# Kernel optimization log

Measured on AMD Instinct MI355X. Metric: run time of the kernel, lower is better.

The kernel has to match this reference:

```python
import math
import jax, jax.numpy as jnp
import numpy as np


def _sinkhorn_attn(q, n):
    """Log-domain Sinkhorn-Knopp, eps=1, max_iter=1, uniform marginals.
    cost C = -q @ q^T, so M = (-C + u + v)/eps = S + u + v with S = q q^T.
    Returns transport plan pi = exp(S + u_i + v_j).  q: [B, n, d]."""
    S = jnp.einsum('bnd,bmd->bnm', q, q)            # [B, n, n]
    log_marg = -math.log(n)                          # log(1/n)
    u = log_marg - jax.nn.logsumexp(S, axis=-1)      # [B, n] row update
    v = log_marg - jax.nn.logsumexp(S + u[..., :, None], axis=-2)  # [B, n] col update
    return jnp.exp(S + u[..., :, None] + v[..., None, :])


def reference(x, row_embed, col_embed):
    # x: [B, d, H, W]; row_embed/col_embed: [len_embedding, d//2]
    B, d, H, W = x.shape
    # learned positional embedding: [H, W, d] -> [d, H, W]
    x_emb = col_embed[:W]                             # [W, F]
    y_emb = row_embed[:H]                             # [H, F]
    F = x_emb.shape[-1]
    pos = jnp.concatenate([
        jnp.broadcast_to(x_emb[None, :, :], (H, W, F)),
        jnp.broadcast_to(y_emb[:, None, :], (H, W, F)),
    ], axis=-1).transpose(2, 0, 1)                    # [d, H, W]
    x = x + pos[None]

    n = H * W
    xf = x.reshape(B, d, n).transpose(0, 2, 1)        # [B, n, d] = q = k = v (v unscaled)
    inv_sqrtV = 1.0 / math.sqrt(math.sqrt(d))         # d**-0.25 applied to q and k each
    attn = _sinkhorn_attn(xf * inv_sqrtV, n)          # [B, n, n]
    out = jnp.einsum('bnm,bmd->bnd', attn, xf)        # [B, n, d]
    return out.transpose(0, 2, 1).reshape(B, d, H, W)


def setup_inputs() -> dict:
    key = jax.random.key(0)
    k1, k2, k3 = jax.random.split(key, 3)
    B, d, H, W = 32, 512, 32, 32
    len_emb, F = 32, d // 2
    return {
        'x': jax.random.normal(k1, (B, d, H, W), dtype=jnp.float32),
        'row_embed': jax.random.uniform(k2, (len_emb, F), dtype=jnp.float32),
        'col_embed': jax.random.uniform(k3, (len_emb, F), dtype=jnp.float32),
    }
```

## Files before the change

kernel.cpp:

```cpp
#include <hip/hip_runtime.h>
#include <hip/hip_fp16.h>
#include <math.h>

typedef _Float16 f16;
typedef _Float16 f16x8 __attribute__((ext_vector_type(8)));
typedef _Float16 f16x4 __attribute__((ext_vector_type(4)));
typedef float f32x4 __attribute__((ext_vector_type(4)));

namespace {
constexpr int kB = 32, kD = 512, kN = 1024, kF = 256;
constexpr float kScale = 0.04419417382415922f;
constexpr float kLogMarg = -6.931471805599453f;
constexpr float kMarg = 1.f / 1024.f;
constexpr float kPScale = 16384.f;
constexpr float kPInv = 1.f / 16384.f;
}

__device__ __forceinline__ void gload16(const void* g, void* l) {
  __builtin_amdgcn_global_load_lds(
      (const __attribute__((address_space(1))) void*)g,
      (__attribute__((address_space(3))) void*)l, 16, 0, 0);
}

__global__ __launch_bounds__(256) void k_prep(
    const float* __restrict__ x, const float* __restrict__ re,
    const float* __restrict__ ce, f16* __restrict__ xf,
    f16* __restrict__ xfT, int b0) {
  __shared__ f16 T[64][68];
  const int lb = blockIdx.z;
  const int i0 = blockIdx.x * 64, c0 = blockIdx.y * 64;
  const int t = threadIdx.x;
  const int il = (t & 15) * 4;
  const int cl = t >> 4;
  const size_t xbase = ((size_t)(b0 + lb) * kD) * kN;
#pragma unroll
  for (int p = 0; p < 4; p++) {
    const int c = c0 + cl + 16 * p;
    const int i = i0 + il;
    const float4 xv = *(const float4*)(x + xbase + (size_t)c * kN + i);
    float4 pv;
    if (c < kF) {
      pv.x = ce[((i + 0) & 31) * kF + c];
      pv.y = ce[((i + 1) & 31) * kF + c];
      pv.z = ce[((i + 2) & 31) * kF + c];
      pv.w = ce[((i + 3) & 31) * kF + c];
    } else {
      const float r = re[(i >> 5) * kF + (c - kF)];
      pv.x = r; pv.y = r; pv.z = r; pv.w = r;
    }
    const f16 h0 = (f16)(xv.x + pv.x), h1 = (f16)(xv.y + pv.y);
    const f16 h2 = (f16)(xv.z + pv.z), h3 = (f16)(xv.w + pv.w);
    f16* dT = xfT + ((size_t)lb * kD + c) * kN + i;
    *(f16x4*)dT = (f16x4){h0, h1, h2, h3};
    T[cl + 16 * p][il + 0] = h0; T[cl + 16 * p][il + 1] = h1;
    T[cl + 16 * p][il + 2] = h2; T[cl + 16 * p][il + 3] = h3;
  }
  __syncthreads();
#pragma unroll
  for (int p = 0; p < 4; p++) {
    const int ir = cl + 16 * p;
    const int cc = il;
    const f16 h0 = T[cc + 0][ir], h1 = T[cc + 1][ir];
    const f16 h2 = T[cc + 2][ir], h3 = T[cc + 3][ir];
    f16* dF = xf + ((size_t)lb * kN + i0 + ir) * kD + c0 + cc;
    *(f16x4*)dF = (f16x4){h0, h1, h2, h3};
  }
}

__global__ __launch_bounds__(256) void k_gemm_s(
    const f16* __restrict__ xf, f16* __restrict__ S16,
    float* __restrict__ rp) {
  __shared__ char sm[65536];
  const int nwg = (int)(gridDim.x * gridDim.z);
  const int lin = (int)(blockIdx.x + gridDim.x * blockIdx.z);
  const int wid = (lin & 7) * (nwg >> 3) + (lin >> 3);
  const int bz = wid / 36;
  int qq = wid - bz * 36;
  int by = 0;
  while (qq >= 8 - by) { qq -= 8 - by; by++; }
  const int bx = by + qq;

  const int lb = bz;
  const int i0 = by * 128, j0 = bx * 128;
  const char* base = (const char*)(xf + (size_t)lb * kN * kD);
  const int t = threadIdx.x;
  const int w = t >> 6, lane = t & 63;
  const int m_off = (w >> 1) * 64, n_off = (w & 1) * 64;
  const int quad = lane >> 4, l15 = lane & 15;
  const int swz = (l15 & 7) << 4;

  int srcA[4], srcB[4], ldsw[4];
#pragma unroll
  for (int p = 0; p < 4; p++) {
    const int off = p * 4096 + w * 1024 + lane * 16;
    const int r = off >> 7;
    const int cb = (off & 127) ^ ((r & 7) << 4);
    srcA[p] = (i0 + r) * (kD * 2) + cb;
    srcB[p] = (j0 + r) * (kD * 2) + cb;
    ldsw[p] = p * 4096 + w * 1024;
  }

  f32x4 acc[4][4];
#pragma unroll
  for (int a = 0; a < 4; a++)
#pragma unroll
    for (int b = 0; b < 4; b++) acc[a][b] = (f32x4){0.f, 0.f, 0.f, 0.f};

#pragma unroll
  for (int p = 0; p < 4; p++) gload16(base + srcA[p], sm + ldsw[p]);
#pragma unroll
  for (int p = 0; p < 4; p++) gload16(base + srcB[p], sm + 16384 + ldsw[p]);
  __syncthreads();

#pragma unroll
  for (int tt = 0; tt < 8; tt++) {
    const int cur = tt & 1, nxt = cur ^ 1;
    if (tt + 1 < 8) {
      const int k0b = (tt + 1) * 128;
#pragma unroll
      for (int p = 0; p < 4; p++)
        gload16(base + srcA[p] + k0b, sm + (nxt << 15) + ldsw[p]);
#pragma unroll
      for (int p = 0; p < 4; p++)
        gload16(base + srcB[p] + k0b, sm + (nxt << 15) + 16384 + ldsw[p]);
    }
    const char* bA = sm + (cur << 15);
    const char* bB = bA + 16384;
#pragma unroll
    for (int kk = 0; kk < 2; kk++) {
      f16x8 af[4], bf[4];
#pragma unroll
      for (int q = 0; q < 4; q++)
        af[q] = *(const f16x8*)(bA + (m_off + 16 * q + l15) * 128 +
                                ((kk * 64 + quad * 16) ^ swz));
#pragma unroll
      for (int q = 0; q < 4; q++)
        bf[q] = *(const f16x8*)(bB + (n_off + 16 * q + l15) * 128 +
                                ((kk * 64 + quad * 16) ^ swz));
#pragma unroll
      for (int qa = 0; qa < 4; qa++)
#pragma unroll
        for (int qb = 0; qb < 4; qb++)
          acc[qa][qb] = __builtin_amdgcn_mfma_f32_16x16x32_f16(
              af[qa], bf[qb], acc[qa][qb], 0, 0, 0);
    }
    __syncthreads();
  }

  f16* Sb = S16 + (size_t)lb * kN * kN;
  const int jt2 = bx * 2 + (w & 1);
  float* rpb = rp + ((size_t)lb * 16 + jt2) * kN + i0 + m_off;
  const bool offd = (bx != by);
  float cs[4] = {0.f, 0.f, 0.f, 0.f};
#pragma unroll
  for (int qa = 0; qa < 4; qa++) {
    const int i = i0 + m_off + 16 * qa + quad * 4;
    float rs[4] = {0.f, 0.f, 0.f, 0.f};
#pragma unroll
    for (int qb = 0; qb < 4; qb++) {
      const int j = j0 + n_off + 16 * qb + l15;
      f16 h4[4];
#pragma unroll
      for (int r = 0; r < 4; r++) {
        const f16 h = (f16)(acc[qa][qb][r] * kScale);
        Sb[(size_t)(i + r) * kN + j] = h;
        h4[r] = h;
        const float e = __expf((float)h);
        rs[r] += e;
        cs[qb] += e;
      }
      if (offd)
        *(f16x4*)(Sb + (size_t)j * kN + i) = (f16x4){h4[0], h4[1], h4[2], h4[3]};
    }
#pragma unroll
    for (int r = 0; r < 4; r++) {
      float s = rs[r];
      s += __shfl_xor(s, 1);
      s += __shfl_xor(s, 2);
      s += __shfl_xor(s, 4);
      s += __shfl_xor(s, 8);
      if (l15 == 0) rpb[16 * qa + 4 * quad + r] = s;
    }
  }
  if (offd) {
    float* rpm = rp + ((size_t)lb * 16 + (by * 2 + (w >> 1))) * kN;
#pragma unroll
    for (int qb = 0; qb < 4; qb++) {
      float s = cs[qb];
      s += __shfl_xor(s, 16);
      s += __shfl_xor(s, 32);
      if (quad == 0) rpm[j0 + n_off + 16 * qb + l15] = s;
    }
  }
}

__global__ __launch_bounds__(256) void k_u(
    const float* __restrict__ rp, float* __restrict__ u) {
  const int lb = blockIdx.y;
  const int i = blockIdx.x * 256 + threadIdx.x;
  const float* r = rp + (size_t)lb * 16 * kN + i;
  float s = 0.f;
#pragma unroll
  for (int t = 0; t < 16; t++) s += r[(size_t)t * kN];
  u[lb * kN + i] = kLogMarg - __logf(s);
}

__global__ __launch_bounds__(256) void k_cs(
    const f16* __restrict__ S16, const float* __restrict__ u,
    float* __restrict__ cp) {
  const int lb = blockIdx.z;
  const int seg = blockIdx.y;
  const int j = threadIdx.x * 4;
  const f16* Sb = S16 + (size_t)lb * kN * kN + (size_t)(seg * 64) * kN + j;
  const float* ub = u + lb * kN + seg * 64;
  float s0 = 0.f, s1 = 0.f, s2 = 0.f, s3 = 0.f;
#pragma unroll 8
  for (int r = 0; r < 64; r++) {
    const f16x4 v = *(const f16x4*)(Sb + (size_t)r * kN);
    const float ur = ub[r];
    s0 += __expf((float)v[0] + ur);
    s1 += __expf((float)v[1] + ur);
    s2 += __expf((float)v[2] + ur);
    s3 += __expf((float)v[3] + ur);
  }
  float4 o = {s0, s1, s2, s3};
  *(float4*)(cp + ((size_t)lb * 16 + seg) * kN + j) = o;
}

__global__ __launch_bounds__(256) void k_v(
    const float* __restrict__ cp, float* __restrict__ ev) {
  const int lb = blockIdx.y;
  const int j = blockIdx.x * 256 + threadIdx.x;
  const float* c = cp + (size_t)lb * 16 * kN + j;
  float s = 0.f;
#pragma unroll
  for (int r = 0; r < 16; r++) s += c[(size_t)r * kN];
  ev[lb * kN + j] = kMarg / s;
}

__global__ __launch_bounds__(256) void k_pt(
    const f16* __restrict__ S16, const float* __restrict__ u,
    const float* __restrict__ ev, f16* __restrict__ t16) {
  const int row = blockIdx.x;
  const float ui = u[row];
  const f16* Sr = S16 + (size_t)row * kN;
  const float* evb = ev + (size_t)(row >> 10) * kN;
  f16* Tr = t16 + (size_t)row * kN;
  const int j = threadIdx.x * 4;
  const f16x4 s = *(const f16x4*)(Sr + j);
  const float4 e = *(const float4*)(evb + j);
  f16x4 o;
  o[0] = (f16)(__expf((float)s[0] + ui) * e.x * kPScale);
  o[1] = (f16)(__expf((float)s[1] + ui) * e.y * kPScale);
  o[2] = (f16)(__expf((float)s[2] + ui) * e.z * kPScale);
  o[3] = (f16)(__expf((float)s[3] + ui) * e.w * kPScale);
  *(f16x4*)(Tr + j) = o;
}

#define AF_READ(q)                                                          \
  _Pragma("unroll")                                                         \
  for (int pa = 0; pa < 2; pa++)                                            \
    _Pragma("unroll")                                                       \
    for (int kk = 0; kk < 2; kk++)                                          \
      af[pa][kk] = *(const f16x8*)(bA + (m_off + 32*(q) + 16*pa + l15)*128  \
                                   + ((kk*64 + quad*16) ^ swz));

#define MFMA_PH(q)                                                          \
  __builtin_amdgcn_s_setprio(1);                                            \
  _Pragma("unroll")                                                         \
  for (int pa = 0; pa < 2; pa++)                                            \
    _Pragma("unroll")                                                       \
    for (int qb = 0; qb < 4; qb++)                                          \
      _Pragma("unroll")                                                     \
      for (int kk = 0; kk < 2; kk++)                                        \
        acc[2*(q)+pa][qb] = __builtin_amdgcn_mfma_f32_16x16x32_f16(         \
            af[pa][kk], bf[qb][kk], acc[2*(q)+pa][qb], 0, 0, 0);            \
  __builtin_amdgcn_s_setprio(0);

__global__ __launch_bounds__(512) void k_gemm_o(
    const f16* __restrict__ xfT, const f16* __restrict__ P,
    float* __restrict__ out, int b0) {
  __shared__ char sm[131072];
  const int nwg = (int)(gridDim.x * gridDim.y * gridDim.z);
  const int lin = (int)(blockIdx.x +
                        gridDim.x * (blockIdx.y + gridDim.y * blockIdx.z));
  const int wid = (lin & 7) * (nwg >> 3) + (lin >> 3);
  const int bx = wid & 3, by = (wid >> 2) & 1, bz = wid >> 3;

  const int lb = bz;
  const int i0 = bx * 256, c0 = by * 256;
  const char* Ab = (const char*)(xfT + (size_t)lb * kD * kN);
  const char* Bb = (const char*)(P + (size_t)lb * kN * kN);
  const int t = threadIdx.x;
  const int w = t >> 6, lane = t & 63;
  const int wm = w >> 2, wn = w & 3;
  const int m_off = wm * 128, n_off = wn * 64;
  const int quad = lane >> 4, l15 = lane & 15;
  const int swz = (l15 & 7) << 4;

  int srcA[4], srcB[4], ldsw[4];
#pragma unroll
  for (int p = 0; p < 4; p++) {
    const int off = p * 8192 + t * 16;
    const int r = off >> 7;
    const int cb = (off & 127) ^ ((r & 7) << 4);
    srcA[p] = (c0 + r) * (kN * 2) + cb;
    srcB[p] = (i0 + r) * (kN * 2) + cb;
    ldsw[p] = p * 8192 + w * 1024;
  }

#pragma unroll
  for (int p = 0; p < 4; p++) gload16(Bb + srcB[p], sm + 65536 + ldsw[p]);
  gload16(Ab + srcA[0], sm + ldsw[0]);
  gload16(Ab + srcA[2], sm + ldsw[2]);
  gload16(Ab + srcA[1], sm + ldsw[1]);
  gload16(Ab + srcA[3], sm + ldsw[3]);
#pragma unroll
  for (int p = 0; p < 4; p++)
    gload16(Bb + srcB[p] + 128, sm + 65536 + 32768 + ldsw[p]);
  f32x4 acc[8][4];
#pragma unroll
  for (int a = 0; a < 8; a++)
#pragma unroll
    for (int b = 0; b < 4; b++) acc[a][b] = (f32x4){0.f, 0.f, 0.f, 0.f};
  asm volatile("s_waitcnt vmcnt(6)" ::: "memory");
  __builtin_amdgcn_s_barrier();
  __builtin_amdgcn_sched_barrier(0);

#pragma unroll
  for (int tt = 0; tt < 16; tt++) {
    const int cur = tt & 1, nxt = cur ^ 1;
    const char* bA = sm + cur * 32768;
    const char* bB = sm + 65536 + cur * 32768;
    char* wA = sm + nxt * 32768;
    char* wB = sm + 65536 + cur * 32768;
    const int kA = (tt + 1) * 128, kBB = (tt + 2) * 128;
    f16x8 bf[4][2], af[2][2];
#pragma unroll
    for (int qb = 0; qb < 4; qb++)
#pragma unroll
      for (int kk = 0; kk < 2; kk++)
        bf[qb][kk] = *(const f16x8*)(bB + (n_off + 16 * qb + l15) * 128 +
                                     ((kk * 64 + quad * 16) ^ swz));
    AF_READ(0)
    asm volatile("s_waitcnt lgkmcnt(0)" ::: "memory");
    __builtin_amdgcn_sched_barrier(0);
    __builtin_amdgcn_s_barrier();
    MFMA_PH(0)
    if (tt + 1 < 16) {
      gload16(Ab + srcA[0] + kA, wA + ldsw[0]);
      gload16(Ab + srcA[2] + kA, wA + ldsw[2]);
    }
    AF_READ(1)
    __builtin_amdgcn_s_barrier();
    MFMA_PH(1)
    if (tt == 15) { asm volatile("s_waitcnt vmcnt(0)" ::: "memory"); }
    else          { asm volatile("s_waitcnt vmcnt(6)" ::: "memory"); }
    __builtin_amdgcn_s_barrier();
    __builtin_amdgcn_sched_barrier(0);
    AF_READ(2)
    __builtin_amdgcn_s_barrier();
    MFMA_PH(2)
    if (tt + 1 < 16) {
      gload16(Ab + srcA[1] + kA, wA + ldsw[1]);
      gload16(Ab + srcA[3] + kA, wA + ldsw[3]);
    }
    if (tt + 2 < 16) {
#pragma unroll
      for (int p = 0; p < 4; p++)
        gload16(Bb + srcB[p] + kBB, wB + ldsw[p]);
    }
    AF_READ(3)
    __builtin_amdgcn_s_barrier();
    MFMA_PH(3)
    if (tt + 2 < 16)      { asm volatile("s_waitcnt vmcnt(6)" ::: "memory"); }
    else if (tt + 1 < 16) { asm volatile("s_waitcnt vmcnt(2)" ::: "memory"); }
    __builtin_amdgcn_s_barrier();
    __builtin_amdgcn_sched_barrier(0);
  }

  float* ob = out + ((size_t)(b0 + lb) * kD) * kN;
#pragma unroll
  for (int qa = 0; qa < 8; qa++) {
    const int c = c0 + m_off + 16 * qa + quad * 4;
#pragma unroll
    for (int qb = 0; qb < 4; qb++) {
      const int i = i0 + n_off + 16 * qb + l15;
#pragma unroll
      for (int r = 0; r < 4; r++)
        ob[(size_t)(c + r) * kN + i] = acc[qa][qb][r] * kPInv;
    }
  }
}

extern "C" void kernel_launch(void* const* d_in, const int* in_sizes, int n_in,
                              void* d_out, int out_size, void* d_ws, size_t ws_size,
                              hipStream_t stream) {
  const float* x = (const float*)d_in[0];
  const float* re = (const float*)d_in[1];
  const float* ce = (const float*)d_in[2];
  float* out = (float*)d_out;

  char* wsb = (char*)d_ws;
  const size_t perb = 2097152ull + 1048576 + 1048576 + 2097152 +
                      4096 + 4096 + 65536 + 65536;
  int G = (int)(ws_size / perb);
  if (G >= 32) G = 32;
  else if (G >= 16) G = 16;
  else if (G >= 8) G = 8;
  else if (G >= 4) G = 4;
  else if (G < 1) G = 1;
  f16* S16 = (f16*)wsb;
  f16* xf = (f16*)(wsb + (size_t)G * 2097152);
  f16* xfT = (f16*)((char*)xf + (size_t)G * 1048576);
  f16* t16 = (f16*)((char*)xfT + (size_t)G * 1048576);
  float* u = (float*)((char*)t16 + (size_t)G * 2097152);
  float* ev = u + (size_t)G * kN;
  float* rp = ev + (size_t)G * kN;
  float* cp = rp + (size_t)G * 16 * kN;

  for (int b0 = 0; b0 < kB; b0 += G) {
    const int g = (kB - b0 < G) ? (kB - b0) : G;
    k_prep<<<dim3(16, 8, g), 256, 0, stream>>>(x, re, ce, xf, xfT, b0);
    k_gemm_s<<<dim3(36, 1, g), 256, 0, stream>>>(xf, S16, rp);
    k_u<<<dim3(4, g), 256, 0, stream>>>(rp, u);
    k_cs<<<dim3(1, 16, g), 256, 0, stream>>>(S16, u, cp);
    k_v<<<dim3(4, g), 256, 0, stream>>>(cp, ev);
    k_pt<<<g * kN, 256, 0, stream>>>(S16, u, ev, t16);
    k_gemm_o<<<dim3(4, 2, g), 512, 0, stream>>>(xfT, t16, out, b0);
  }
}
```

Before: 238.0 us.

## Fold row and column logsumexp reductions into column-sum and plan kernels

Removes the separate k_u and k_v launches by computing the row normaliser u inside k_cs (64 rows per block, kept in shared memory) and the column scale ev inside k_pt (each block re-reduces the 16 column partials). k_pt is also restructured from one block per row to one block per 64-row segment, looping over rows. This cuts two launches and round trips through global memory per batch group. In exchange, k_pt now has far fewer blocks (16 per batch) and each one repeats the column reduction, so parallelism for this memory-bound pass drops.

```diff
diff --git a/kernel.cpp b/kernel.cpp
--- a/kernel.cpp
+++ b/kernel.cpp
@@ -194,30 +194,30 @@
   }
 }
 
-__global__ __launch_bounds__(256) void k_u(
-    const float* __restrict__ rp, float* __restrict__ u) {
-  const int lb = blockIdx.y;
-  const int i = blockIdx.x * 256 + threadIdx.x;
-  const float* r = rp + (size_t)lb * 16 * kN + i;
-  float s = 0.f;
-#pragma unroll
-  for (int t = 0; t < 16; t++) s += r[(size_t)t * kN];
-  u[lb * kN + i] = kLogMarg - __logf(s);
-}
-
 __global__ __launch_bounds__(256) void k_cs(
-    const f16* __restrict__ S16, const float* __restrict__ u,
-    float* __restrict__ cp) {
+    const f16* __restrict__ S16, const float* __restrict__ rp,
+    float* __restrict__ u, float* __restrict__ cp) {
+  __shared__ float us[64];
   const int lb = blockIdx.z;
   const int seg = blockIdx.y;
-  const int j = threadIdx.x * 4;
+  const int tid = threadIdx.x;
+  if (tid < 64) {
+    const float* r = rp + (size_t)lb * 16 * kN + seg * 64 + tid;
+    float s = 0.f;
+#pragma unroll
+    for (int t = 0; t < 16; t++) s += r[(size_t)t * kN];
+    const float uu = kLogMarg - __logf(s);
+    us[tid] = uu;
+    u[lb * kN + seg * 64 + tid] = uu;
+  }
+  __syncthreads();
+  const int j = tid * 4;
   const f16* Sb = S16 + (size_t)lb * kN * kN + (size_t)(seg * 64) * kN + j;
-  const float* ub = u + lb * kN + seg * 64;
   float s0 = 0.f, s1 = 0.f, s2 = 0.f, s3 = 0.f;
 #pragma unroll 8
   for (int r = 0; r < 64; r++) {
     const f16x4 v = *(const f16x4*)(Sb + (size_t)r * kN);
-    const float ur = ub[r];
+    const float ur = us[r];
     s0 += __expf((float)v[0] + ur);
     s1 += __expf((float)v[1] + ur);
     s2 += __expf((float)v[2] + ur);
@@ -227,34 +227,38 @@
   *(float4*)(cp + ((size_t)lb * 16 + seg) * kN + j) = o;
 }
 
-__global__ __launch_bounds__(256) void k_v(
-    const float* __restrict__ cp, float* __restrict__ ev) {
-  const int lb = blockIdx.y;
-  const int j = blockIdx.x * 256 + threadIdx.x;
-  const float* c = cp + (size_t)lb * 16 * kN + j;
-  float s = 0.f;
-#pragma unroll
-  for (int r = 0; r < 16; r++) s += c[(size_t)r * kN];
-  ev[lb * kN + j] = kMarg / s;
-}
-
 __global__ __launch_bounds__(256) void k_pt(
     const f16* __restrict__ S16, const float* __restrict__ u,
-    const float* __restrict__ ev, f16* __restrict__ t16) {
-  const int row = blockIdx.x;
-  const float ui = u[row];
-  const f16* Sr = S16 + (size_t)row * kN;
-  const float* evb = ev + (size_t)(row >> 10) * kN;
-  f16* Tr = t16 + (size_t)row * kN;
-  const int j = threadIdx.x * 4;
-  const f16x4 s = *(const f16x4*)(Sr + j);
-  const float4 e = *(const float4*)(evb + j);
-  f16x4 o;
-  o[0] = (f16)(__expf((float)s[0] + ui) * e.x * kPScale);
-  o[1] = (f16)(__expf((float)s[1] + ui) * e.y * kPScale);
-  o[2] = (f16)(__expf((float)s[2] + ui) * e.z * kPScale);
-  o[3] = (f16)(__expf((float)s[3] + ui) * e.w * kPScale);
-  *(f16x4*)(Tr + j) = o;
+    const float* __restrict__ cp, f16* __restrict__ t16) {
+  __shared__ float us[64];
+  const int seg = blockIdx.x;
+  const int lb = blockIdx.y;
+  const int tid = threadIdx.x;
+  const int j = tid * 4;
+  const float* c = cp + (size_t)lb * 16 * kN + j;
+  float s0 = 0.f, s1 = 0.f, s2 = 0.f, s3 = 0.f;
+#pragma unroll
+  for (int r = 0; r < 16; r++) {
+    const float4 v = *(const float4*)(c + (size_t)r * kN);
+    s0 += v.x; s1 += v.y; s2 += v.z; s3 += v.w;
+  }
+  const float e0 = kMarg / s0, e1 = kMarg / s1;
+  const float e2 = kMarg / s2, e3 = kMarg / s3;
+  if (tid < 64) us[tid] = u[lb * kN + seg * 64 + tid];
+  __syncthreads();
+  const f16* Sb = S16 + (size_t)lb * kN * kN + (size_t)(seg * 64) * kN + j;
+  f16* Tb = t16 + (size_t)lb * kN * kN + (size_t)(seg * 64) * kN + j;
+#pragma unroll 4
+  for (int r = 0; r < 64; r++) {
+    const f16x4 v = *(const f16x4*)(Sb + (size_t)r * kN);
+    const float ur = us[r];
+    f16x4 o;
+    o[0] = (f16)(__expf((float)v[0] + ur) * e0 * kPScale);
+    o[1] = (f16)(__expf((float)v[1] + ur) * e1 * kPScale);
+    o[2] = (f16)(__expf((float)v[2] + ur) * e2 * kPScale);
+    o[3] = (f16)(__expf((float)v[3] + ur) * e3 * kPScale);
+    *(f16x4*)(Tb + (size_t)r * kN) = o;
+  }
 }
 
 #define AF_READ(q)                                                          \
@@ -403,7 +407,7 @@
 
   char* wsb = (char*)d_ws;
   const size_t perb = 2097152ull + 1048576 + 1048576 + 2097152 +
-                      4096 + 4096 + 65536 + 65536;
+                      4096 + 65536 + 65536;
   int G = (int)(ws_size / perb);
   if (G >= 32) G = 32;
   else if (G >= 16) G = 16;
@@ -415,18 +419,15 @@
   f16* xfT = (f16*)((char*)xf + (size_t)G * 1048576);
   f16* t16 = (f16*)((char*)xfT + (size_t)G * 1048576);
   float* u = (float*)((char*)t16 + (size_t)G * 2097152);
-  float* ev = u + (size_t)G * kN;
-  float* rp = ev + (size_t)G * kN;
+  float* rp = u + (size_t)G * kN;
   float* cp = rp + (size_t)G * 16 * kN;
 
   for (int b0 = 0; b0 < kB; b0 += G) {
     const int g = (kB - b0 < G) ? (kB - b0) : G;
     k_prep<<<dim3(16, 8, g), 256, 0, stream>>>(x, re, ce, xf, xfT, b0);
     k_gemm_s<<<dim3(36, 1, g), 256, 0, stream>>>(xf, S16, rp);
-    k_u<<<dim3(4, g), 256, 0, stream>>>(rp, u);
-    k_cs<<<dim3(1, 16, g), 256, 0, stream>>>(S16, u, cp);
-    k_v<<<dim3(4, g), 256, 0, stream>>>(cp, ev);
-    k_pt<<<g * kN, 256, 0, stream>>>(S16, u, ev, t16);
+    k_cs<<<dim3(1, 16, g), 256, 0, stream>>>(S16, rp, u, cp);
+    k_pt<<<dim3(16, g), 256, 0, stream>>>(S16, u, cp, t16);
     k_gemm_o<<<dim3(4, 2, g), 512, 0, stream>>>(xfT, t16, out, b0);
   }
 }
```

Result: faster. 232.0 us (-2.5%).
